# Kernel tuning notes

Measured on AMD Instinct MI355X. Metric: run time of the kernel, lower is better.

## Reference

```python
import jax, jax.numpy as jnp
import numpy as np

MAX_SEQLEN = 2048  # static max sequence length (flash varlen APIs take this as a host arg)


def setup_inputs() -> dict:
    key = jax.random.key(0)
    k1, k2, k3 = jax.random.split(key, 3)
    T, H, D = 8192, 8, 128
    B = 4
    q = jax.random.normal(k1, (T, H, D), dtype=jnp.float32)
    k = jax.random.normal(k2, (T, H, D), dtype=jnp.float32)
    v = jax.random.normal(k3, (T, H, D), dtype=jnp.float32)
    cu = (jnp.arange(B + 1, dtype=jnp.int32) * (T // B))  # [0,2048,4096,6144,8192]
    return {"q": q, "k": k, "v": v, "cu_seqlens_q": cu, "cu_seqlens_k": cu}


def reference(q, k, v, cu_seqlens_q, cu_seqlens_k):
    """Varlen (ragged) multi-head attention, non-causal (flash_attn varlen default).

    q,k,v: [T, H, D] packed over sequences; cu_seqlens: [B+1] boundaries.
    Gathers each sequence into a padded [B, S, H, D] layout, computes
    per-sequence softmax(q k^T / sqrt(D)) v with padding masked, then
    scatters back to packed [T, H, D].
    """
    T, H, D = q.shape
    B = cu_seqlens_q.shape[0] - 1
    S = MAX_SEQLEN
    scale = 1.0 / jnp.sqrt(jnp.asarray(D, q.dtype))

    pos = jnp.arange(S)
    q_start = cu_seqlens_q[:-1]
    k_start = cu_seqlens_k[:-1]
    q_len = jnp.diff(cu_seqlens_q)  # [B]
    k_len = jnp.diff(cu_seqlens_k)

    q_idx = jnp.clip(q_start[:, None] + pos[None, :], 0, T - 1)  # [B, S]
    k_idx = jnp.clip(k_start[:, None] + pos[None, :], 0, T - 1)
    q_valid = pos[None, :] < q_len[:, None]  # [B, S]
    k_valid = pos[None, :] < k_len[:, None]

    qb = q[q_idx]  # [B, S, H, D]
    kb = k[k_idx]
    vb = v[k_idx]

    scores = jnp.einsum('bqhd,bkhd->bhqk', qb, kb) * scale  # [B, H, S, S]
    neg = jnp.asarray(-1e30, scores.dtype)
    scores = jnp.where(k_valid[:, None, None, :], scores, neg)
    attn = jax.nn.softmax(scores, axis=-1)
    ob = jnp.einsum('bhqk,bkhd->bqhd', attn, vb)  # [B, S, H, D]

    # zero padded query rows, then scatter-add back to packed layout
    ob = jnp.where(q_valid[:, :, None, None], ob, 0.0)
    out = jnp.zeros_like(q).at[q_idx.reshape(-1)].add(ob.reshape(B * S, H, D))
    return out
```

## Files before the change

### kernel.cpp

```cpp
#include <hip/hip_runtime.h>
#include <hip/hip_bf16.h>
#include <stdint.h>

#define HH 8
#define DD 128
#define MAXSEQ 2048
#define QBLK 128

typedef float f32x16 __attribute__((ext_vector_type(16)));
typedef short s16x8 __attribute__((ext_vector_type(8)));

__device__ __forceinline__ unsigned short f2bf(float x) {
  union { float f; uint32_t u; } v; v.f = x;
  uint32_t u = v.u;
  return (unsigned short)((u + 0x7FFFu + ((u >> 16) & 1u)) >> 16);
}

__global__ void zero_rows(const int* __restrict__ cuq, float* __restrict__ out, int T, int B) {
  const int t = blockIdx.x * blockDim.x + threadIdx.x;
  if (t >= T) return;
  bool covered = false;
  for (int b = 0; b < B; ++b) {
    const int s = cuq[b];
    const int len = min(cuq[b + 1] - s, MAXSEQ);
    if (t >= s && t < s + len) covered = true;
  }
  if (!covered) {
    float4* p = (float4*)(out + (size_t)t * HH * DD);
#pragma unroll 4
    for (int i = 0; i < HH * DD / 4; ++i) p[i] = float4{0.f, 0.f, 0.f, 0.f};
  }
}

__global__ void kvconv(const float* __restrict__ k, const float* __restrict__ v,
                       unsigned short* __restrict__ kb2, unsigned short* __restrict__ vb2, int T) {
  const int TBc = T >> 5;
  const int total = TBc * HH * 512;
  int u = blockIdx.x * blockDim.x + threadIdx.x;
  if (u < total) {
    const int lp = u & 63;
    const int key = lp & 31, hi = lp >> 5;
    int r = u >> 6;
    const int s = r & 7; r >>= 3;
    const int tb = r % TBc;
    const int h = r / TBc;
    const int t = tb * 32 + key;
    const int d = s * 16 + hi * 8;
    const float* src = k + ((size_t)t * HH + h) * DD + d;
    float4 a = *(const float4*)src;
    float4 c = *(const float4*)(src + 4);
    union { unsigned short us[8]; uint4 q; } w;
    w.us[0] = f2bf(a.x); w.us[1] = f2bf(a.y); w.us[2] = f2bf(a.z); w.us[3] = f2bf(a.w);
    w.us[4] = f2bf(c.x); w.us[5] = f2bf(c.y); w.us[6] = f2bf(c.z); w.us[7] = f2bf(c.w);
    *(uint4*)(kb2 + (size_t)u * 8) = w.q;
  } else if ((u -= total) < total) {
    const int lo = u & 31;
    const int hi = (u >> 5) & 1;
    const int i = (u >> 6) & 7;
    const int dt = i & 3, ks2 = i >> 2;
    int r = u >> 9;
    const int tb = r % TBc;
    const int h = r / TBc;
    const int t0 = tb * 32 + ks2 * 16 + hi * 8;
    const int d = dt * 32 + lo;
    union { unsigned short us[8]; uint4 q; } w;
#pragma unroll
    for (int j = 0; j < 8; ++j)
      w.us[j] = f2bf(v[((size_t)(t0 + j) * HH + h) * DD + d]);
    *(uint4*)(vb2 + (size_t)u * 8) = w.q;
  }
}

__global__ __launch_bounds__(256, 2)
void attn_main(const float* __restrict__ q,
               const unsigned short* __restrict__ kb2,
               const unsigned short* __restrict__ vb2,
               const int* __restrict__ cuq,
               const int* __restrict__ cuk,
               float* __restrict__ out,
               int T, int BH) {
  const int TBc = T >> 5;
  const int bid = blockIdx.x;
  const int bh = bid % BH;
  const int qt = bid / BH;
  const int b = bh / HH, h = bh % HH;
  const int qs = cuq[b], qe = cuq[b + 1];
  const int ks = cuk[b], ke = cuk[b + 1];
  const int nq = min(qe - qs, MAXSEQ);
  const int nk = min(ke - ks, MAXSEQ);
  if (qt * QBLK >= nq || nk <= 0) return;

  const int tid = threadIdx.x;
  const int wave = tid >> 6;
  const int lane = tid & 63;
  const int lo = lane & 31;
  const int hi = lane >> 5;

  const int kb32 = ks >> 5;
  const unsigned short* kb2h = kb2 + (size_t)h * TBc * 4096;
  const unsigned short* vb2h = vb2 + (size_t)h * TBc * 4096;

  const float SC = (1.0f / 11.313708498984761f) * 1.4426950408889634f;
  const int qrow = qt * QBLK + wave * 32 + lo;
  const int qg = qs + min(qrow, nq - 1);
  const float* qp = q + ((size_t)qg * HH + h) * DD;
  s16x8 qf[8];
#pragma unroll
  for (int s = 0; s < 8; ++s) {
    const float* p0 = qp + s * 16 + hi * 8;
    float4 a = *(const float4*)(p0);
    float4 c = *(const float4*)(p0 + 4);
    union { unsigned short us[8]; s16x8 v; } u;
    u.us[0] = f2bf(a.x * SC); u.us[1] = f2bf(a.y * SC);
    u.us[2] = f2bf(a.z * SC); u.us[3] = f2bf(a.w * SC);
    u.us[4] = f2bf(c.x * SC); u.us[5] = f2bf(c.y * SC);
    u.us[6] = f2bf(c.z * SC); u.us[7] = f2bf(c.w * SC);
    qf[s] = u.v;
  }

  f32x16 Oa[4];
#pragma unroll
  for (int i = 0; i < 4; ++i)
#pragma unroll
    for (int r = 0; r < 16; ++r) Oa[i][r] = 0.0f;

  float l_run = 0.0f;
  const int nkt = (nk + 31) / 32;

  s16x8 kf[8], vf[8];
  f32x16 stA, stB;
  uint32_t pu[8];

  auto loadK = [&](int stile) {
    const unsigned short* base = kb2h + (size_t)stile * 4096 + lane * 8;
#pragma unroll
    for (int s = 0; s < 8; ++s)
      kf[s] = *(const s16x8*)(base + s * 512);
  };
  auto loadV = [&](int stile) {
    const unsigned short* base = vb2h + (size_t)stile * 4096 + lane * 8;
#pragma unroll
    for (int i = 0; i < 8; ++i)
      vf[i] = *(const s16x8*)(base + i * 512);
  };

  auto QK = [&](f32x16& st) {
#pragma unroll
    for (int r = 0; r < 16; ++r) st[r] = 0.0f;
    __builtin_amdgcn_s_setprio(1);
#pragma unroll
    for (int s = 0; s < 8; ++s)
      st = __builtin_amdgcn_mfma_f32_32x32x16_bf16(kf[s], qf[s], st, 0, 0, 0);
    __builtin_amdgcn_s_setprio(0);
  };

  auto SMPACK = [&](f32x16& st) {
    float p[16];
#pragma unroll
    for (int r = 0; r < 16; ++r) p[r] = __builtin_amdgcn_exp2f(st[r]);
    float s01 = (p[0] + p[1]) + (p[2] + p[3]);
    float s23 = (p[4] + p[5]) + (p[6] + p[7]);
    float s45 = (p[8] + p[9]) + (p[10] + p[11]);
    float s67 = (p[12] + p[13]) + (p[14] + p[15]);
    l_run += (s01 + s23) + (s45 + s67);
    uint32_t ownu[8];
#pragma unroll
    for (int c = 0; c < 4; ++c) {
      uint32_t w0, w1;
      asm("v_cvt_pk_bf16_f32 %0, %1, %2" : "=v"(w0) : "v"(p[4 * c + 0]), "v"(p[4 * c + 1]));
      asm("v_cvt_pk_bf16_f32 %0, %1, %2" : "=v"(w1) : "v"(p[4 * c + 2]), "v"(p[4 * c + 3]));
      ownu[c * 2 + 0] = w0;
      ownu[c * 2 + 1] = w1;
    }
#pragma unroll
    for (int ks2 = 0; ks2 < 2; ++ks2) {
      uint32_t a0 = ownu[4 * ks2 + 0], b0 = ownu[4 * ks2 + 2];
      uint32_t a1 = ownu[4 * ks2 + 1], b1 = ownu[4 * ks2 + 3];
      asm("v_permlane32_swap_b32 %0, %1" : "+v"(a0), "+v"(b0));
      asm("v_permlane32_swap_b32 %0, %1" : "+v"(a1), "+v"(b1));
      pu[4 * ks2 + 0] = a0; pu[4 * ks2 + 1] = a1;
      pu[4 * ks2 + 2] = b0; pu[4 * ks2 + 3] = b1;
    }
  };

  auto PV = [&]() {
    __builtin_amdgcn_s_setprio(1);
#pragma unroll
    for (int ks2 = 0; ks2 < 2; ++ks2) {
      union { uint32_t u[4]; s16x8 v; } pv_;
      pv_.u[0] = pu[4 * ks2 + 0]; pv_.u[1] = pu[4 * ks2 + 1];
      pv_.u[2] = pu[4 * ks2 + 2]; pv_.u[3] = pu[4 * ks2 + 3];
#pragma unroll
      for (int dt = 0; dt < 4; ++dt)
        Oa[dt] = __builtin_amdgcn_mfma_f32_32x32x16_bf16(pv_.v, vf[ks2 * 4 + dt], Oa[dt], 0, 0, 0);
    }
    __builtin_amdgcn_s_setprio(0);
  };

  auto MASK = [&](f32x16& st) {
    const int lim = nk - (nkt - 1) * 32;
    if (lim < 32) {
#pragma unroll
      for (int r = 0; r < 16; ++r) {
        const int base = (r & 3) + 8 * (r >> 2) + 4 * hi;
        if (base >= lim) st[r] = -__builtin_inff();
      }
    }
  };

  auto ITER = [&](int t, f32x16& stPrev, f32x16& stCur) {
    loadV(kb32 + t - 1);
    SMPACK(stPrev);
    QK(stCur);
    if (t + 1 < nkt) loadK(kb32 + t + 1);
    PV();
  };

  auto EPI = [&](f32x16& stLast) {
    loadV(kb32 + nkt - 1);
    MASK(stLast);
    SMPACK(stLast);
    PV();
  };

  loadK(kb32);
  QK(stA);
  if (nkt > 1) loadK(kb32 + 1);

  int t = 1;
  for (; t + 1 < nkt; t += 2) {
    ITER(t, stA, stB);
    ITER(t + 1, stB, stA);
  }
  if (t < nkt) { ITER(t, stA, stB); EPI(stB); }
  else EPI(stA);

  l_run += __shfl_xor(l_run, 32);
  const float linv = 1.0f / l_run;
#pragma unroll
  for (int r = 0; r < 16; ++r) {
    const int src = (r & 3) + 8 * (r >> 2) + 4 * hi;
    const float li = __shfl(linv, src);
    const int qirow = qt * QBLK + wave * 32 + src;
    if (qirow < nq) {
      float* op = out + ((size_t)(qs + qirow) * HH + h) * DD;
      op[0 * 32 + lo] = Oa[0][r] * li;
      op[1 * 32 + lo] = Oa[1][r] * li;
      op[2 * 32 + lo] = Oa[2][r] * li;
      op[3 * 32 + lo] = Oa[3][r] * li;
    }
  }
}

extern "C" void kernel_launch(void* const* d_in, const int* in_sizes, int n_in,
                              void* d_out, int out_size, void* d_ws, size_t ws_size,
                              hipStream_t stream) {
  const float* q = (const float*)d_in[0];
  const float* k = (const float*)d_in[1];
  const float* v = (const float*)d_in[2];
  const int* cuq = (const int*)d_in[3];
  const int* cuk = (const int*)d_in[4];
  float* out = (float*)d_out;
  const int T = in_sizes[0] / (HH * DD);
  const int B = in_sizes[3] - 1;

  unsigned short* kb2 = (unsigned short*)d_ws;
  unsigned short* vb2 = kb2 + (size_t)T * HH * DD;
  const size_t need = (size_t)T * HH * DD * 2 * 2;
  if (ws_size < need) return;

  {
    zero_rows<<<(T + 255) / 256, 256, 0, stream>>>(cuq, out, T, B);
  }
  {
    const int total = (T >> 5) * HH * 512;
    kvconv<<<(2 * total + 255) / 256, 256, 0, stream>>>(k, v, kb2, vb2, T);
  }
  {
    const int BH = B * HH;
    const int scap = MAXSEQ < T ? MAXSEQ : T;
    const int qtiles = (scap + QBLK - 1) / QBLK;
    attn_main<<<BH * qtiles, 256, 0, stream>>>(q, kb2, vb2, cuq, cuk, out, T, BH);
  }
}
```

Before: 115.0 us.

## Interleave QK and PV MFMAs with split accumulators in attention loop

Restructures the flash-attention inner loop so the QK^T MFMA chain for the next key tile is interleaved one-for-one with the PV MFMAs for the previous tile. QK uses two independent accumulators that are summed before softmax, which breaks the serial dependency chain of 8 MFMAs. The previous double-buffered stA/stB unrolled ITER scheme is replaced by a single loop that defers loadV until after the MFMAs. This is meant to hide MFMA latency and dependency stalls, at the cost of an extra vector add and more accumulator registers, which could lower occupancy.

```diff
diff --git a/kernel.cpp b/kernel.cpp
--- a/kernel.cpp
+++ b/kernel.cpp
@@ -128,7 +128,7 @@
   const int nkt = (nk + 31) / 32;
 
   s16x8 kf[8], vf[8];
-  f32x16 stA, stB;
+  f32x16 cQ0, cQ1;
   uint32_t pu[8];
 
   auto loadK = [&](int stile) {
@@ -144,17 +144,18 @@
       vf[i] = *(const s16x8*)(base + i * 512);
   };
 
-  auto QK = [&](f32x16& st) {
-#pragma unroll
-    for (int r = 0; r < 16; ++r) st[r] = 0.0f;
-    __builtin_amdgcn_s_setprio(1);
-#pragma unroll
-    for (int s = 0; s < 8; ++s)
-      st = __builtin_amdgcn_mfma_f32_32x32x16_bf16(kf[s], qf[s], st, 0, 0, 0);
-    __builtin_amdgcn_s_setprio(0);
-  };
-
-  auto SMPACK = [&](f32x16& st) {
+  auto SMPACK = [&](bool domask) {
+    f32x16 st = cQ0 + cQ1;
+    if (domask) {
+      const int lim = nk - (nkt - 1) * 32;
+      if (lim < 32) {
+#pragma unroll
+        for (int r = 0; r < 16; ++r) {
+          const int base = (r & 3) + 8 * (r >> 2) + 4 * hi;
+          if (base >= lim) st[r] = -__builtin_inff();
+        }
+      }
+    }
     float p[16];
 #pragma unroll
     for (int r = 0; r < 16; ++r) p[r] = __builtin_amdgcn_exp2f(st[r]);
@@ -183,57 +184,65 @@
     }
   };
 
-  auto PV = [&]() {
+  auto ZEROQ = [&]() {
+#pragma unroll
+    for (int r = 0; r < 16; ++r) { cQ0[r] = 0.0f; cQ1[r] = 0.0f; }
+  };
+
+  loadK(kb32);
+  ZEROQ();
+  __builtin_amdgcn_s_setprio(1);
+#pragma unroll
+  for (int s = 0; s < 8; s += 2) {
+    cQ0 = __builtin_amdgcn_mfma_f32_32x32x16_bf16(kf[s], qf[s], cQ0, 0, 0, 0);
+    cQ1 = __builtin_amdgcn_mfma_f32_32x32x16_bf16(kf[s + 1], qf[s + 1], cQ1, 0, 0, 0);
+  }
+  __builtin_amdgcn_s_setprio(0);
+  loadV(kb32);
+  if (nkt > 1) loadK(kb32 + 1);
+
+  for (int t = 1; t < nkt; ++t) {
+    SMPACK(false);
+    union { uint32_t u[4]; s16x8 v; } pv0, pv1;
+    pv0.u[0] = pu[0]; pv0.u[1] = pu[1]; pv0.u[2] = pu[2]; pv0.u[3] = pu[3];
+    pv1.u[0] = pu[4]; pv1.u[1] = pu[5]; pv1.u[2] = pu[6]; pv1.u[3] = pu[7];
+    ZEROQ();
     __builtin_amdgcn_s_setprio(1);
-#pragma unroll
-    for (int ks2 = 0; ks2 < 2; ++ks2) {
-      union { uint32_t u[4]; s16x8 v; } pv_;
-      pv_.u[0] = pu[4 * ks2 + 0]; pv_.u[1] = pu[4 * ks2 + 1];
-      pv_.u[2] = pu[4 * ks2 + 2]; pv_.u[3] = pu[4 * ks2 + 3];
-#pragma unroll
-      for (int dt = 0; dt < 4; ++dt)
-        Oa[dt] = __builtin_amdgcn_mfma_f32_32x32x16_bf16(pv_.v, vf[ks2 * 4 + dt], Oa[dt], 0, 0, 0);
-    }
+    cQ0 = __builtin_amdgcn_mfma_f32_32x32x16_bf16(kf[0], qf[0], cQ0, 0, 0, 0);
+    Oa[0] = __builtin_amdgcn_mfma_f32_32x32x16_bf16(pv0.v, vf[0], Oa[0], 0, 0, 0);
+    cQ1 = __builtin_amdgcn_mfma_f32_32x32x16_bf16(kf[1], qf[1], cQ1, 0, 0, 0);
+    Oa[1] = __builtin_amdgcn_mfma_f32_32x32x16_bf16(pv0.v, vf[1], Oa[1], 0, 0, 0);
+    cQ0 = __builtin_amdgcn_mfma_f32_32x32x16_bf16(kf[2], qf[2], cQ0, 0, 0, 0);
+    Oa[2] = __builtin_amdgcn_mfma_f32_32x32x16_bf16(pv0.v, vf[2], Oa[2], 0, 0, 0);
+    cQ1 = __builtin_amdgcn_mfma_f32_32x32x16_bf16(kf[3], qf[3], cQ1, 0, 0, 0);
+    Oa[3] = __builtin_amdgcn_mfma_f32_32x32x16_bf16(pv0.v, vf[3], Oa[3], 0, 0, 0);
+    cQ0 = __builtin_amdgcn_mfma_f32_32x32x16_bf16(kf[4], qf[4], cQ0, 0, 0, 0);
+    Oa[0] = __builtin_amdgcn_mfma_f32_32x32x16_bf16(pv1.v, vf[4], Oa[0], 0, 0, 0);
+    cQ1 = __builtin_amdgcn_mfma_f32_32x32x16_bf16(kf[5], qf[5], cQ1, 0, 0, 0);
+    Oa[1] = __builtin_amdgcn_mfma_f32_32x32x16_bf16(pv1.v, vf[5], Oa[1], 0, 0, 0);
+    cQ0 = __builtin_amdgcn_mfma_f32_32x32x16_bf16(kf[6], qf[6], cQ0, 0, 0, 0);
+    Oa[2] = __builtin_amdgcn_mfma_f32_32x32x16_bf16(pv1.v, vf[6], Oa[2], 0, 0, 0);
+    cQ1 = __builtin_amdgcn_mfma_f32_32x32x16_bf16(kf[7], qf[7], cQ1, 0, 0, 0);
+    Oa[3] = __builtin_amdgcn_mfma_f32_32x32x16_bf16(pv1.v, vf[7], Oa[3], 0, 0, 0);
     __builtin_amdgcn_s_setprio(0);
-  };
-
-  auto MASK = [&](f32x16& st) {
-    const int lim = nk - (nkt - 1) * 32;
-    if (lim < 32) {
-#pragma unroll
-      for (int r = 0; r < 16; ++r) {
-        const int base = (r & 3) + 8 * (r >> 2) + 4 * hi;
-        if (base >= lim) st[r] = -__builtin_inff();
-      }
-    }
-  };
-
-  auto ITER = [&](int t, f32x16& stPrev, f32x16& stCur) {
-    loadV(kb32 + t - 1);
-    SMPACK(stPrev);
-    QK(stCur);
+    loadV(kb32 + t);
     if (t + 1 < nkt) loadK(kb32 + t + 1);
-    PV();
-  };
-
-  auto EPI = [&](f32x16& stLast) {
-    loadV(kb32 + nkt - 1);
-    MASK(stLast);
-    SMPACK(stLast);
-    PV();
-  };
-
-  loadK(kb32);
-  QK(stA);
-  if (nkt > 1) loadK(kb32 + 1);
-
-  int t = 1;
-  for (; t + 1 < nkt; t += 2) {
-    ITER(t, stA, stB);
-    ITER(t + 1, stB, stA);
-  }
-  if (t < nkt) { ITER(t, stA, stB); EPI(stB); }
-  else EPI(stA);
+  }
+
+  SMPACK(true);
+  {
+    union { uint32_t u[4]; s16x8 v; } pv0, pv1;
+    pv0.u[0] = pu[0]; pv0.u[1] = pu[1]; pv0.u[2] = pu[2]; pv0.u[3] = pu[3];
+    pv1.u[0] = pu[4]; pv1.u[1] = pu[5]; pv1.u[2] = pu[6]; pv1.u[3] = pu[7];
+    __builtin_amdgcn_s_setprio(1);
+#pragma unroll
+    for (int dt = 0; dt < 4; ++dt)
+      Oa[dt] = __builtin_amdgcn_mfma_f32_32x32x16_bf16(pv0.v, vf[dt], Oa[dt], 0, 0, 0);
+#pragma unroll
+    for (int dt = 0; dt < 4; ++dt)
+      Oa[dt] = __builtin_amdgcn_mfma_f32_32x32x16_bf16(pv1.v, vf[4 + dt], Oa[dt], 0, 0, 0);
+    __builtin_amdgcn_s_setprio(0);
+  }
 
   l_run += __shfl_xor(l_run, 32);
   const float linv = 1.0f / l_run;
```

Measured after the change: 125.9 us. 1.09x slower.
